# Kernel tuning notes

Hardware: AMD Instinct MI355X
Metric: run time of the kernel (lower is better)

The kernel has to match this reference:

```python
import jax, jax.numpy as jnp
import numpy as np

N = 2048      # num graph nodes (activities + places)
D = 256       # embedding_size
C = 3 * D     # cat_embedding_size
V = 2         # num variants
L = 16        # activities per variant
E = 16 * N    # edges for the encoder GNN
DEG_P = 0.0156  # adjacency density (~32 out-degree)


def setup_inputs() -> dict:
    key = jax.random.key(0)
    ks = jax.random.split(key, 6)
    embeddings = jax.random.normal(ks[0], (N, D), dtype=jnp.float32)
    W_self = jax.random.normal(ks[1], (D, D), dtype=jnp.float32) * 0.05
    W_nbr = jax.random.normal(ks[2], (D, D), dtype=jnp.float32) * 0.05
    b = jnp.zeros((D,), dtype=jnp.float32)
    variants = jax.random.randint(ks[3], (V, L), 0, N, dtype=jnp.int32)
    original = (jax.random.uniform(ks[4], (N, N)) < DEG_P).astype(jnp.int32)
    edge_index = jax.random.randint(ks[5], (2, E), 0, N, dtype=jnp.int32)
    return {"embeddings": embeddings, "W_self": W_self, "W_nbr": W_nbr, "b": b,
            "variants": variants, "original": original, "edge_index": edge_index}


def _forward(embeddings, W_self, W_nbr, b, variants, original, edge_index):
    n, d = embeddings.shape
    c = 3 * d
    dt = embeddings.dtype
    adj = original.astype(dt)              # [N,N]; adj[i,j]=1 iff edge i->j (forward star = row)
    src_e, dst_e = edge_index[0], edge_index[1]

    def encoder(x):
        # SecondEncoder approximated as one GCN-style message-passing layer
        msg = jax.ops.segment_sum(x[src_e], dst_e, num_segments=n)
        return jax.nn.relu(x @ W_self + msg @ W_nbr + b)

    def run_variant(acts):  # acts: [L] int32
        onehot = jax.nn.one_hot(acts, n, dtype=dt)                # [L,N]
        incl = jnp.flip(jnp.cumsum(jnp.flip(onehot, 0), 0), 0)    # sum_{j>=i} onehot[j]
        present_later = ((incl - onehot) > 0).astype(dt)          # set of nodes in acts[i+1:]

        def step(carry, inp):
            emb, pi, summary = carry
            a, plater = inp
            followers = adj[a]                                    # forward star of activity a
            has = jnp.any(followers > 0)
            adj_m = adj * plater[None, :]                         # edges into later-in-variant activities
            dest_cnt = adj_m.sum(axis=1)                          # |destination set| per candidate place
            dst_all = adj_m @ emb                                 # summed destination embeddings, [N,D]
            mask = jnp.where(has, ((followers > 0) & (dest_cnt > 0)).astype(dt), 0.0)
            # cat = (place_f, src_f, dst_f) per considered place
            cat = jnp.concatenate(
                [emb, jnp.broadcast_to(emb[a][None, :], emb.shape), dst_all], axis=1) * mask[:, None]
            pi = pi + cat                                         # places_info[place] += cat
            # prev_embedding_summary += places_info[place] for each considered place
            summary = summary + (mask[:, None] * pi).sum(axis=0)
            # places_info[considered] += prev_embedding_summary
            pi = pi + mask[:, None] * summary[None, :]
            emb = jnp.where(has, encoder(emb), emb)               # encoder skipped when no followers
            return (emb, pi, summary), None

        init = (embeddings, jnp.zeros((n, c), dt), jnp.zeros((c,), dt))
        (_, pi, _), _ = jax.lax.scan(step, init, (acts, present_later))
        return pi

    # variant shuffle in the original is irrelevant: embeddings reset each variant
    # and final_places_info is a sum over variants.
    return jax.vmap(run_variant)(variants).sum(axis=0)


def reference(embeddings, W_self, W_nbr, b, variants, original, edge_index):
    return _forward(embeddings, W_self, W_nbr, b, variants, original, edge_index)
```

## Files before the change

kernel.cpp:

```cpp
#include <hip/hip_runtime.h>

#define N 2048
#define D 256
#define C 768
#define V 2
#define L 16
#define NSTATE 15
#define NAPP 14
#define TCAP 256
#define FCAP 64

typedef __attribute__((ext_vector_type(8))) short bf16x8;
typedef __attribute__((ext_vector_type(4))) float f32x4;

__device__ __forceinline__ ushort bf16_rn(float x) {
  unsigned u = __float_as_uint(x);
  u += 0x7FFFu + ((u >> 16) & 1u);
  return (ushort)(u >> 16);
}
__device__ __forceinline__ float bf16_f(ushort h) {
  return __uint_as_float(((unsigned)h) << 16);
}

__device__ __forceinline__ size_t a_addr(int row, int k) {
  return ((size_t)(row >> 5) * 4 + (k >> 6)) * 2048 + (row & 31) * 64 + (k & 63);
}
__device__ __forceinline__ size_t wt_addr(int n, int k) {
  return ((size_t)(n >> 5) * 4 + (k >> 6)) * 2048 + (n & 31) * 64 + (k & 63);
}

__global__ __launch_bounds__(256) void k_init(
    const float* __restrict__ emb, const float* __restrict__ Ws,
    const float* __restrict__ Wn, float* __restrict__ states0,
    ushort* __restrict__ WtHi, ushort* __restrict__ WtLo,
    ushort* __restrict__ A0hi, ushort* __restrict__ A0lo,
    float* __restrict__ out, int* __restrict__ fillpos) {
  size_t i = (size_t)blockIdx.x * 256 + threadIdx.x;
  size_t stride = (size_t)gridDim.x * 256;
  for (size_t x = i; x < (size_t)N * D; x += stride) {
    float v = emb[x];
    states0[x] = v;
    ushort h = bf16_rn(v);
    ushort l = bf16_rn(v - bf16_f(h));
    size_t a = a_addr((int)(x >> 8), (int)(x & 255));
    A0hi[a] = h;
    A0lo[a] = l;
  }
  for (size_t x = i; x < (size_t)512 * 256; x += stride) {
    int n = (int)(x >> 8), k = (int)(x & 255);
    float v = (n < 256) ? Ws[(size_t)k * 256 + n] : Wn[(size_t)k * 256 + (n - 256)];
    ushort h = bf16_rn(v);
    size_t a = wt_addr(n, k);
    WtHi[a] = h;
    WtLo[a] = bf16_rn(v - bf16_f(h));
  }
  for (size_t x = i; x < (size_t)N * C; x += stride) out[x] = 0.f;
  for (size_t x = i; x < N; x += stride) fillpos[x] = 0;
}

__global__ __launch_bounds__(256) void k_degA(
    const int* __restrict__ ei, int E, int* __restrict__ fillpos,
    const int* __restrict__ adj, const int* __restrict__ variants,
    int* __restrict__ stepP, int* __restrict__ stepDm,
    int* __restrict__ stepCnt, int* __restrict__ hasG, int* __restrict__ tlG) {
  __shared__ int tl_sh[16];
  __shared__ int foll[FCAP], fbits[FCAP];
  __shared__ int sh_tc, sh_fcnt, sh_ecnt;
  int t = threadIdx.x;
  if (blockIdx.x < 128) {
    for (int e = blockIdx.x * 256 + t; e < E; e += 128 * 256)
      atomicAdd(&fillpos[ei[E + e]], 1);
    return;
  }
  int vi = blockIdx.x - 128;
  int v = vi / L, i = vi % L;
  int a = variants[vi];
  if (t == 0) {
    int cnt = 0;
    for (int j = i + 1; j < L; j++) {
      int x = variants[v * L + j];
      bool dup = false;
      for (int q = 0; q < cnt; q++) if (tl_sh[q] == x) dup = true;
      if (!dup) tl_sh[cnt++] = x;
    }
    sh_tc = cnt;
    sh_fcnt = 0;
    sh_ecnt = 0;
    for (int q = 0; q < cnt; q++) tlG[vi * 16 + q] = tl_sh[q];
  }
  __syncthreads();
  for (int p = t; p < N; p += 256) {
    if (adj[(size_t)a * N + p] != 0) {
      int f = atomicAdd(&sh_fcnt, 1);
      if (f < FCAP) foll[f] = p;
    }
  }
  __syncthreads();
  int fc = sh_fcnt < FCAP ? sh_fcnt : FCAP;
  int tc = sh_tc;
  for (int x = t; x < fc; x += 256) fbits[x] = 0;
  __syncthreads();
  for (int x = t; x < fc * tc; x += 256) {
    int fi = x / tc, q = x - fi * tc;
    if (adj[(size_t)foll[fi] * N + tl_sh[q]] != 0) atomicOr(&fbits[fi], 1 << q);
  }
  __syncthreads();
  for (int fi = t; fi < fc; fi += 256) {
    int bits = fbits[fi];
    if (bits) {
      int e = atomicAdd(&sh_ecnt, 1);
      stepP[vi * FCAP + e] = foll[fi];
      stepDm[vi * FCAP + e] = bits;
    }
  }
  __syncthreads();
  if (t == 0) {
    stepCnt[vi] = sh_ecnt;
    hasG[vi] = (sh_fcnt > 0);
  }
}

__global__ __launch_bounds__(256) void k_scan(int* __restrict__ fillpos,
                                              int* __restrict__ row_ptr) {
  __shared__ int part[256];
  __shared__ int base[257];
  int t = threadIdx.x;
  int v[8];
  int s = 0;
  for (int j = 0; j < 8; j++) { v[j] = fillpos[t * 8 + j]; s += v[j]; }
  part[t] = s;
  __syncthreads();
  if (t == 0) {
    int acc = 0;
    for (int q = 0; q < 256; q++) { base[q] = acc; acc += part[q]; }
    base[256] = acc;
  }
  __syncthreads();
  int acc = base[t];
  for (int j = 0; j < 8; j++) {
    row_ptr[t * 8 + j] = acc;
    fillpos[t * 8 + j] = acc;
    acc += v[j];
  }
  if (t == 255) row_ptr[N] = base[256];
}

__global__ __launch_bounds__(256) void k_fillB(
    const int* __restrict__ ei, int E, int* __restrict__ fillpos,
    int* __restrict__ csr_src,
    const int* __restrict__ stepP, const int* __restrict__ stepDm,
    const int* __restrict__ stepCnt, const int* __restrict__ hasG,
    int* __restrict__ entP, int* __restrict__ entPrev, int* __restrict__ entDm,
    int* __restrict__ offsG, int* __restrict__ kidxG, int* __restrict__ cmatG,
    int* __restrict__ lastPG, int* __restrict__ lastIG, int* __restrict__ lastMG,
    int* __restrict__ cntG) {
  __shared__ int pmask[N];
  __shared__ int sP[16][FCAP];
  __shared__ int sDm[16][FCAP];
  __shared__ int cnt[16], offs[17];
  __shared__ int cmat_sh[256];
  __shared__ int sh_u;
  int t = threadIdx.x;
  if (blockIdx.x < 128) {
    for (int e = blockIdx.x * 256 + t; e < E; e += 128 * 256) {
      int dst = ei[E + e];
      int pos = atomicAdd(&fillpos[dst], 1);
      csr_src[pos] = ei[e];
    }
    return;
  }
  int v = blockIdx.x - 128;
  for (int p = t; p < N; p += 256) pmask[p] = 0;
  for (int x = t; x < 256; x += 256) cmat_sh[x] = 0;
  if (t < 16) cnt[t] = stepCnt[v * L + t];
  if (t == 0) sh_u = 0;
  __syncthreads();
  if (t == 0) {
    int acc = 0;
    for (int i = 0; i < 16; i++) {
      offs[i] = acc < TCAP ? acc : TCAP;
      acc += cnt[i];
    }
    offs[16] = acc < TCAP ? acc : TCAP;
    cntG[v * 2 + 0] = offs[16];
    int k = 0;
    for (int i = 0; i < L; i++) {
      kidxG[v * 16 + i] = k;
      if (hasG[v * L + i]) k++;
    }
  }
  for (int x = t; x < 16 * FCAP; x += 256) {
    int i = x >> 6, f = x & 63;
    if (f < stepCnt[v * L + i]) {
      int p = stepP[(v * L + i) * FCAP + f];
      sP[i][f] = p;
      sDm[i][f] = stepDm[(v * L + i) * FCAP + f];
      atomicOr(&pmask[p], 1 << i);
    }
  }
  __syncthreads();
  for (int x = t; x < 16 * FCAP; x += 256) {
    int i = x >> 6, f = x & 63;
    if (f < cnt[i]) {
      int e = offs[i] + f;
      if (e < TCAP) {
        int p = sP[i][f];
        entP[v * TCAP + e] = p;
        entDm[v * TCAP + e] = sDm[i][f];
        int m = pmask[p] & ((1 << i) - 1);
        int prev = -1;
        if (m) {
          int j = 31 - __clz(m);
          int cj = cnt[j];
          for (int f2 = 0; f2 < cj; f2++)
            if (sP[j][f2] == p) { prev = offs[j] + f2; break; }
        }
        entPrev[v * TCAP + e] = prev;
      }
    }
  }
  __syncthreads();
  for (int p = t; p < N; p += 256) {
    int m = pmask[p];
    if (m) {
      int u = atomicAdd(&sh_u, 1);
      int j = 31 - __clz(m);
      int li = -1;
      int cj = cnt[j];
      for (int f2 = 0; f2 < cj; f2++)
        if (sP[j][f2] == p) { li = offs[j] + f2; break; }
      lastPG[v * TCAP + u] = p;
      lastIG[v * TCAP + u] = li;
      lastMG[v * TCAP + u] = m;
      int mm = m;
      while (mm) {
        int bi = __ffs(mm) - 1; mm &= mm - 1;
        int m2 = m & ((1 << bi) - 1);
        while (m2) {
          int bj = __ffs(m2) - 1; m2 &= m2 - 1;
          atomicAdd(&cmat_sh[bi * 16 + bj], 1);
        }
      }
    }
  }
  __syncthreads();
  if (t == 0) cntG[v * 2 + 1] = sh_u;
  for (int x = t; x < 256; x += 256) cmatG[v * 256 + x] = cmat_sh[x];
  for (int x = t; x < 17; x += 256) offsG[v * 17 + x] = offs[x];
}

__global__ __launch_bounds__(256) void k_gemm(
    const ushort* __restrict__ Ah, const ushort* __restrict__ Al,
    const ushort* __restrict__ Wh_g, const ushort* __restrict__ Wl_g,
    float* __restrict__ Z) {
  __shared__ __align__(16) ushort Ash[2][32][72], Asl[2][32][72];
  __shared__ __align__(16) ushort Wsh[2][32][72], Wsl[2][32][72];
  const int tid = threadIdx.x, wave = tid >> 6, lane = tid & 63;
  const int quad = lane >> 4, l16 = lane & 15;
  const int wr = wave >> 1, wc = wave & 1;
  const int mb = blockIdx.x, nb = blockIdx.y;
  const int sr = tid >> 3, sc = (tid & 7) * 8;

  f32x4 acc = {0.f, 0.f, 0.f, 0.f};
  size_t abase = (size_t)mb * 4 * 2048 + (size_t)tid * 8;
  size_t wbase = (size_t)nb * 4 * 2048 + (size_t)tid * 8;
  {
    uint4 ra  = *(const uint4*)&Ah[abase];
    uint4 rl  = *(const uint4*)&Al[abase];
    uint4 rwh = *(const uint4*)&Wh_g[wbase];
    uint4 rwl = *(const uint4*)&Wl_g[wbase];
    *(uint4*)&Ash[0][sr][sc] = ra;
    *(uint4*)&Asl[0][sr][sc] = rl;
    *(uint4*)&Wsh[0][sr][sc] = rwh;
    *(uint4*)&Wsl[0][sr][sc] = rwl;
  }
  __syncthreads();
#pragma unroll
  for (int c = 0; c < 4; c++) {
    const int rb = c & 1;
    uint4 ra, rl, rwh, rwl;
    if (c < 3) {
      size_t o = (size_t)(c + 1) * 2048;
      ra  = *(const uint4*)&Ah[abase + o];
      rl  = *(const uint4*)&Al[abase + o];
      rwh = *(const uint4*)&Wh_g[wbase + o];
      rwl = *(const uint4*)&Wl_g[wbase + o];
    }
#pragma unroll
    for (int kf = 0; kf < 2; kf++) {
      int ko = kf * 32 + quad * 8;
      bf16x8 a_h = *(const bf16x8*)&Ash[rb][wr * 16 + l16][ko];
      bf16x8 a_l = *(const bf16x8*)&Asl[rb][wr * 16 + l16][ko];
      bf16x8 w_h = *(const bf16x8*)&Wsh[rb][wc * 16 + l16][ko];
      bf16x8 w_l = *(const bf16x8*)&Wsl[rb][wc * 16 + l16][ko];
      acc = __builtin_amdgcn_mfma_f32_16x16x32_bf16(a_h, w_h, acc, 0, 0, 0);
      acc = __builtin_amdgcn_mfma_f32_16x16x32_bf16(a_h, w_l, acc, 0, 0, 0);
      acc = __builtin_amdgcn_mfma_f32_16x16x32_bf16(a_l, w_h, acc, 0, 0, 0);
    }
    if (c < 3) {
      const int wb = rb ^ 1;
      *(uint4*)&Ash[wb][sr][sc] = ra;
      *(uint4*)&Asl[wb][sr][sc] = rl;
      *(uint4*)&Wsh[wb][sr][sc] = rwh;
      *(uint4*)&Wsl[wb][sr][sc] = rwl;
      __syncthreads();
    }
  }
  int col = nb * 32 + wc * 16 + l16;
  int row0 = mb * 32 + wr * 16 + quad * 4;
#pragma unroll
  for (int r = 0; r < 4; r++)
    Z[(size_t)(row0 + r) * 512 + col] = acc[r];
}

__global__ __launch_bounds__(256) void k_comb(
    const float* __restrict__ Z, const float* __restrict__ bias,
    const int* __restrict__ row_ptr, const int* __restrict__ csr_src,
    float* __restrict__ stnext, ushort* __restrict__ NAh,
    ushort* __restrict__ NAl) {
  int row = blockIdx.x * 4 + (threadIdx.x >> 6);
  int lane = threadIdx.x & 63;
  const float4* Zp = (const float4*)Z;
  float4 acc = Zp[(size_t)row * 128 + lane];
  float4 acc2 = {0.f, 0.f, 0.f, 0.f};
  int e0 = row_ptr[row], e1 = row_ptr[row + 1];
  int e = e0;
  for (; e + 1 < e1; e += 2) {
    int s0 = csr_src[e], s1 = csr_src[e + 1];
    float4 x0 = Zp[(size_t)s0 * 128 + 64 + lane];
    float4 x1 = Zp[(size_t)s1 * 128 + 64 + lane];
    acc.x += x0.x; acc.y += x0.y; acc.z += x0.z; acc.w += x0.w;
    acc2.x += x1.x; acc2.y += x1.y; acc2.z += x1.z; acc2.w += x1.w;
  }
  if (e < e1) {
    float4 x0 = Zp[(size_t)csr_src[e] * 128 + 64 + lane];
    acc.x += x0.x; acc.y += x0.y; acc.z += x0.z; acc.w += x0.w;
  }
  float4 bv = ((const float4*)bias)[lane];
  float v0 = fmaxf(acc.x + acc2.x + bv.x, 0.f);
  float v1 = fmaxf(acc.y + acc2.y + bv.y, 0.f);
  float v2 = fmaxf(acc.z + acc2.z + bv.z, 0.f);
  float v3 = fmaxf(acc.w + acc2.w + bv.w, 0.f);
  *(float4*)(stnext + (size_t)row * D + lane * 4) = make_float4(v0, v1, v2, v3);
  ushort h0 = bf16_rn(v0), h1 = bf16_rn(v1), h2 = bf16_rn(v2), h3 = bf16_rn(v3);
  size_t ca = a_addr(row, lane * 4);
  *(ushort4*)&NAh[ca] = make_ushort4(h0, h1, h2, h3);
  *(ushort4*)&NAl[ca] = make_ushort4(
      bf16_rn(v0 - bf16_f(h0)), bf16_rn(v1 - bf16_f(h1)),
      bf16_rn(v2 - bf16_f(h2)), bf16_rn(v3 - bf16_f(h3)));
}

#define PI_LDS_BYTES (TCAP * 64 * 4 + 16 * 64 * 4 + 3 * TCAP * 4 + 17 * 4 + 16 * 4 + 256 * 4)
__global__ __launch_bounds__(64) void k_pi(
    const float* __restrict__ states, float* __restrict__ out,
    const int* __restrict__ variants,
    const int* __restrict__ entP, const int* __restrict__ entPrev,
    const int* __restrict__ entDm, const int* __restrict__ offsG,
    const int* __restrict__ kidxG, const int* __restrict__ tlG,
    const int* __restrict__ cmatG, const int* __restrict__ lastPG,
    const int* __restrict__ lastIG, const int* __restrict__ lastMG,
    const int* __restrict__ cntG) {
  extern __shared__ __align__(16) float smf[];
  float* catb = smf;
  float* S_lds = catb + TCAP * 64;
  int* eP  = (int*)(S_lds + 16 * 64);
  int* ePr = eP + TCAP;
  int* eDm = ePr + TCAP;
  int* offs = eDm + TCAP;
  int* kidx = offs + 17;
  int* tl = kidx + 16;
  int v = blockIdx.x / 12, cgi = blockIdx.x % 12;
  int grp = cgi >> 2;
  int lane = threadIdx.x;
  int cl = (cgi & 3) * 64 + lane;
  int col = cgi * 64 + lane;

  int T = cntG[v * 2 + 0], U = cntG[v * 2 + 1];
  for (int x = lane; x < T; x += 64) {
    eP[x] = entP[v * TCAP + x];
    ePr[x] = entPrev[v * TCAP + x];
    eDm[x] = entDm[v * TCAP + x];
  }
  for (int x = lane; x < 17; x += 64) offs[x] = offsG[v * 17 + x];
  if (lane < 16) kidx[lane] = kidxG[v * 16 + lane];
  for (int x = lane; x < 256; x += 64) tl[x] = tlG[v * 256 + x];
  __syncthreads();

  for (int i = 0; i < L; i++) {
    int kk = kidx[i]; if (kk > NSTATE - 1) kk = NSTATE - 1;
    const float* embS = states + (size_t)kk * N * D;
    int o0 = offs[i], o1 = offs[i + 1];
    if (grp == 0) {
      for (int e = o0; e < o1; e++)
        catb[e * 64 + lane] = embS[(size_t)eP[e] * D + cl];
    } else if (grp == 1) {
      float embA = embS[(size_t)variants[v * L + i] * D + cl];
      for (int e = o0; e < o1; e++) catb[e * 64 + lane] = embA;
    } else {
      for (int e = o0; e < o1; e++) {
        float s = 0.f;
        int b = eDm[e];
        while (b) {
          int q = __ffs(b) - 1; b &= b - 1;
          s += embS[(size_t)tl[i * 16 + q] * D + cl];
        }
        catb[e * 64 + lane] = s;
      }
    }
  }
  for (int e = 0; e < T; e++) {
    int pr = ePr[e];
    if (pr >= 0) catb[e * 64 + lane] += catb[pr * 64 + lane];
  }
  float S[16];
  float Sp = 0.f;
#pragma unroll
  for (int i = 0; i < 16; i++) {
    float a = 0.f;
    for (int e = offs[i]; e < offs[i + 1]; e++) a += catb[e * 64 + lane];
    float s = Sp + a;
#pragma unroll
    for (int j = 0; j < 16; j++)
      if (j < i) s += (float)cmatG[v * 256 + i * 16 + j] * S[j];
    S[i] = s;
    S_lds[i * 64 + lane] = s;
    Sp = s;
  }
  for (int u = 0; u < U; u++) {
    int p = lastPG[v * TCAP + u];
    int li = lastIG[v * TCAP + u];
    int m = lastMG[v * TCAP + u];
    float acc = catb[li * 64 + lane];
    while (m) {
      int q = __ffs(m) - 1; m &= m - 1;
      acc += S_lds[q * 64 + lane];
    }
    atomicAdd(&out[(size_t)p * C + col], acc);
  }
}

extern "C" void kernel_launch(void* const* d_in, const int* in_sizes, int n_in,
                              void* d_out, int out_size, void* d_ws, size_t ws_size,
                              hipStream_t stream) {
  const float* emb      = (const float*)d_in[0];
  const float* Ws       = (const float*)d_in[1];
  const float* Wn       = (const float*)d_in[2];
  const float* bias     = (const float*)d_in[3];
  const int*   variants = (const int*)d_in[4];
  const int*   adj      = (const int*)d_in[5];
  const int*   ei       = (const int*)d_in[6];
  const int    E        = in_sizes[6] / 2;
  float* out            = (float*)d_out;

  char* base = (char*)d_ws;
  float* states = (float*)base;            base += (size_t)NSTATE * N * D * 4;
  float* Z      = (float*)base;            base += (size_t)N * 512 * 4;
  ushort* WtHi  = (ushort*)base;           base += (size_t)512 * 256 * 2;
  ushort* WtLo  = (ushort*)base;           base += (size_t)512 * 256 * 2;
  ushort* A0h   = (ushort*)base;           base += (size_t)N * D * 2;
  ushort* A0l   = (ushort*)base;           base += (size_t)N * D * 2;
  ushort* A1h   = (ushort*)base;           base += (size_t)N * D * 2;
  ushort* A1l   = (ushort*)base;           base += (size_t)N * D * 2;
  int* row_ptr  = (int*)base;              base += (N + 1) * 4;
  int* fillpos  = (int*)base;              base += N * 4;
  int* csr_src  = (int*)base;              base += (size_t)E * 4;
  int* stepP    = (int*)base;              base += V * L * FCAP * 4;
  int* stepDm   = (int*)base;              base += V * L * FCAP * 4;
  int* stepCnt  = (int*)base;              base += V * L * 4;
  int* hasG     = (int*)base;              base += V * L * 4;
  int* entP     = (int*)base;              base += V * TCAP * 4;
  int* entPrev  = (int*)base;              base += V * TCAP * 4;
  int* entDm    = (int*)base;              base += V * TCAP * 4;
  int* offsG    = (int*)base;              base += V * 17 * 4;
  int* kidxG    = (int*)base;              base += V * 16 * 4;
  int* tlG      = (int*)base;              base += V * 256 * 4;
  int* cmatG    = (int*)base;              base += V * 256 * 4;
  int* lastPG   = (int*)base;              base += V * TCAP * 4;
  int* lastIG   = (int*)base;              base += V * TCAP * 4;
  int* lastMG   = (int*)base;              base += V * TCAP * 4;
  int* cntG     = (int*)base;              base += V * 2 * 4;

  hipFuncSetAttribute((const void*)k_pi,
                      hipFuncAttributeMaxDynamicSharedMemorySize, PI_LDS_BYTES);

  k_init<<<512, 256, 0, stream>>>(emb, Ws, Wn, states, WtHi, WtLo, A0h, A0l,
                                  out, fillpos);
  k_degA<<<128 + V * L, 256, 0, stream>>>(ei, E, fillpos, adj, variants,
                                          stepP, stepDm, stepCnt, hasG, tlG);
  k_scan<<<1, 256, 0, stream>>>(fillpos, row_ptr);
  k_fillB<<<128 + V, 256, 0, stream>>>(ei, E, fillpos, csr_src, stepP, stepDm,
                                       stepCnt, hasG, entP, entPrev, entDm,
                                       offsG, kidxG, cmatG, lastPG, lastIG,
                                       lastMG, cntG);

  ushort* AH[2] = {A0h, A1h};
  ushort* AL[2] = {A0l, A1l};
  for (int s = 0; s < NAPP; s++) {
    int cur = s & 1, nxt = cur ^ 1;
    k_gemm<<<dim3(64, 16), 256, 0, stream>>>(AH[cur], AL[cur], WtHi, WtLo, Z);
    k_comb<<<N / 4, 256, 0, stream>>>(Z, bias, row_ptr, csr_src,
                                      states + (size_t)(s + 1) * N * D,
                                      AH[nxt], AL[nxt]);
  }
  k_pi<<<V * 12, 64, PI_LDS_BYTES, stream>>>(states, out, variants, entP,
                                             entPrev, entDm, offsG, kidxG, tlG,
                                             cmatG, lastPG, lastIG, lastMG, cntG);
}
```

Before: 376.8 us.

## Parallelize place-info kernel across four waves and unroll neighbor gather by four

```diff
diff --git a/kernel.cpp b/kernel.cpp
--- a/kernel.cpp
+++ b/kernel.cpp
@@ -323,24 +323,31 @@
   const float4* Zp = (const float4*)Z;
   float4 acc = Zp[(size_t)row * 128 + lane];
   float4 acc2 = {0.f, 0.f, 0.f, 0.f};
+  float4 acc3 = {0.f, 0.f, 0.f, 0.f};
+  float4 acc4 = {0.f, 0.f, 0.f, 0.f};
   int e0 = row_ptr[row], e1 = row_ptr[row + 1];
   int e = e0;
-  for (; e + 1 < e1; e += 2) {
+  for (; e + 3 < e1; e += 4) {
     int s0 = csr_src[e], s1 = csr_src[e + 1];
+    int s2 = csr_src[e + 2], s3 = csr_src[e + 3];
     float4 x0 = Zp[(size_t)s0 * 128 + 64 + lane];
     float4 x1 = Zp[(size_t)s1 * 128 + 64 + lane];
+    float4 x2 = Zp[(size_t)s2 * 128 + 64 + lane];
+    float4 x3 = Zp[(size_t)s3 * 128 + 64 + lane];
     acc.x += x0.x; acc.y += x0.y; acc.z += x0.z; acc.w += x0.w;
     acc2.x += x1.x; acc2.y += x1.y; acc2.z += x1.z; acc2.w += x1.w;
-  }
-  if (e < e1) {
+    acc3.x += x2.x; acc3.y += x2.y; acc3.z += x2.z; acc3.w += x2.w;
+    acc4.x += x3.x; acc4.y += x3.y; acc4.z += x3.z; acc4.w += x3.w;
+  }
+  for (; e < e1; e++) {
     float4 x0 = Zp[(size_t)csr_src[e] * 128 + 64 + lane];
     acc.x += x0.x; acc.y += x0.y; acc.z += x0.z; acc.w += x0.w;
   }
   float4 bv = ((const float4*)bias)[lane];
-  float v0 = fmaxf(acc.x + acc2.x + bv.x, 0.f);
-  float v1 = fmaxf(acc.y + acc2.y + bv.y, 0.f);
-  float v2 = fmaxf(acc.z + acc2.z + bv.z, 0.f);
-  float v3 = fmaxf(acc.w + acc2.w + bv.w, 0.f);
+  float v0 = fmaxf(acc.x + acc2.x + acc3.x + acc4.x + bv.x, 0.f);
+  float v1 = fmaxf(acc.y + acc2.y + acc3.y + acc4.y + bv.y, 0.f);
+  float v2 = fmaxf(acc.z + acc2.z + acc3.z + acc4.z + bv.z, 0.f);
+  float v3 = fmaxf(acc.w + acc2.w + acc3.w + acc4.w + bv.w, 0.f);
   *(float4*)(stnext + (size_t)row * D + lane * 4) = make_float4(v0, v1, v2, v3);
   ushort h0 = bf16_rn(v0), h1 = bf16_rn(v1), h2 = bf16_rn(v2), h3 = bf16_rn(v3);
   size_t ca = a_addr(row, lane * 4);
@@ -350,8 +357,9 @@
       bf16_rn(v2 - bf16_f(h2)), bf16_rn(v3 - bf16_f(h3)));
 }
 
-#define PI_LDS_BYTES (TCAP * 64 * 4 + 16 * 64 * 4 + 3 * TCAP * 4 + 17 * 4 + 16 * 4 + 256 * 4)
-__global__ __launch_bounds__(64) void k_pi(
+#define PI_LDS_BYTES (TCAP * 64 * 4 + 16 * 64 * 4 + 16 * 64 * 4 + 256 * 4 + \
+                      3 * TCAP * 4 + 17 * 4 + 16 * 4 + 256 * 4)
+__global__ __launch_bounds__(256) void k_pi(
     const float* __restrict__ states, float* __restrict__ out,
     const int* __restrict__ variants,
     const int* __restrict__ entP, const int* __restrict__ entPrev,
@@ -363,7 +371,9 @@
   extern __shared__ __align__(16) float smf[];
   float* catb = smf;
   float* S_lds = catb + TCAP * 64;
-  int* eP  = (int*)(S_lds + 16 * 64);
+  float* aS = S_lds + 16 * 64;
+  float* cmatf = aS + 16 * 64;
+  int* eP  = (int*)(cmatf + 256);
   int* ePr = eP + TCAP;
   int* eDm = ePr + TCAP;
   int* offs = eDm + TCAP;
@@ -371,19 +381,22 @@
   int* tl = kidx + 16;
   int v = blockIdx.x / 12, cgi = blockIdx.x % 12;
   int grp = cgi >> 2;
-  int lane = threadIdx.x;
+  int tid = threadIdx.x, lane = tid & 63, w = tid >> 6;
   int cl = (cgi & 3) * 64 + lane;
   int col = cgi * 64 + lane;
 
   int T = cntG[v * 2 + 0], U = cntG[v * 2 + 1];
-  for (int x = lane; x < T; x += 64) {
+  for (int x = tid; x < T; x += 256) {
     eP[x] = entP[v * TCAP + x];
     ePr[x] = entPrev[v * TCAP + x];
     eDm[x] = entDm[v * TCAP + x];
   }
-  for (int x = lane; x < 17; x += 64) offs[x] = offsG[v * 17 + x];
-  if (lane < 16) kidx[lane] = kidxG[v * 16 + lane];
-  for (int x = lane; x < 256; x += 64) tl[x] = tlG[v * 256 + x];
+  for (int x = tid; x < 17; x += 256) offs[x] = offsG[v * 17 + x];
+  if (tid < 16) kidx[tid] = kidxG[v * 16 + tid];
+  for (int x = tid; x < 256; x += 256) {
+    tl[x] = tlG[v * 256 + x];
+    cmatf[x] = (float)cmatG[v * 256 + x];
+  }
   __syncthreads();
 
   for (int i = 0; i < L; i++) {
@@ -391,42 +404,57 @@
     const float* embS = states + (size_t)kk * N * D;
     int o0 = offs[i], o1 = offs[i + 1];
     if (grp == 0) {
-      for (int e = o0; e < o1; e++)
+      for (int e = o0 + w; e < o1; e += 4)
         catb[e * 64 + lane] = embS[(size_t)eP[e] * D + cl];
     } else if (grp == 1) {
       float embA = embS[(size_t)variants[v * L + i] * D + cl];
-      for (int e = o0; e < o1; e++) catb[e * 64 + lane] = embA;
+      for (int e = o0 + w; e < o1; e += 4) catb[e * 64 + lane] = embA;
     } else {
-      for (int e = o0; e < o1; e++) {
-        float s = 0.f;
-        int b = eDm[e];
-        while (b) {
-          int q = __ffs(b) - 1; b &= b - 1;
-          s += embS[(size_t)tl[i * 16 + q] * D + cl];
+      for (int e = o0 + w; e < o1; e += 4) {
+        float sa = 0.f;
+        int bm = eDm[e];
+        while (bm) {
+          int q = __ffs(bm) - 1; bm &= bm - 1;
+          sa += embS[(size_t)tl[i * 16 + q] * D + cl];
         }
-        catb[e * 64 + lane] = s;
+        catb[e * 64 + lane] = sa;
       }
     }
   }
-  for (int e = 0; e < T; e++) {
-    int pr = ePr[e];
-    if (pr >= 0) catb[e * 64 + lane] += catb[pr * 64 + lane];
-  }
-  float S[16];
-  float Sp = 0.f;
-#pragma unroll
-  for (int i = 0; i < 16; i++) {
+  __syncthreads();
+  for (int u = w; u < U; u += 4) {
+    int li = lastIG[v * TCAP + u];
+    int len = 0;
+    for (int c2 = li; c2 >= 0; c2 = ePr[c2]) len++;
+    for (int j = 1; j < len; j++) {
+      int c2 = li;
+      for (int k = 0; k < len - 1 - j; k++) c2 = ePr[c2];
+      catb[c2 * 64 + lane] += catb[ePr[c2] * 64 + lane];
+    }
+  }
+  __syncthreads();
+  for (int i = w; i < 16; i += 4) {
     float a = 0.f;
     for (int e = offs[i]; e < offs[i + 1]; e++) a += catb[e * 64 + lane];
-    float s = Sp + a;
+    aS[i * 64 + lane] = a;
+  }
+  __syncthreads();
+  if (w == 0) {
+    float S[16];
+    float Sp = 0.f;
 #pragma unroll
-    for (int j = 0; j < 16; j++)
-      if (j < i) s += (float)cmatG[v * 256 + i * 16 + j] * S[j];
-    S[i] = s;
-    S_lds[i * 64 + lane] = s;
-    Sp = s;
-  }
-  for (int u = 0; u < U; u++) {
+    for (int i = 0; i < 16; i++) {
+      float sv = Sp + aS[i * 64 + lane];
+#pragma unroll
+      for (int j = 0; j < 16; j++)
+        if (j < i) sv += cmatf[i * 16 + j] * S[j];
+      S[i] = sv;
+      S_lds[i * 64 + lane] = sv;
+      Sp = sv;
+    }
+  }
+  __syncthreads();
+  for (int u = w; u < U; u += 4) {
     int p = lastPG[v * TCAP + u];
     int li = lastIG[v * TCAP + u];
     int m = lastMG[v * TCAP + u];
@@ -502,7 +530,8 @@
                                       states + (size_t)(s + 1) * N * D,
                                       AH[nxt], AL[nxt]);
   }
-  k_pi<<<V * 12, 64, PI_LDS_BYTES, stream>>>(states, out, variants, entP,
-                                             entPrev, entDm, offsG, kidxG, tlG,
-                                             cmatG, lastPG, lastIG, lastMG, cntG);
-}
+  k_pi<<<V * 12, 256, PI_LDS_BYTES, stream>>>(states, out, variants, entP,
+                                              entPrev, entDm, offsG, kidxG, tlG,
+                                              cmatG, lastPG, lastIG, lastMG,
+                                              cntG);
+}
```

New measurement: 346.2 us. 8.1% less time.
